# Performance work log

Measured on AMD Instinct MI355X. Metric: run time of the kernel, lower is better.

## Reference

```python
import jax, jax.numpy as jnp
import numpy as np

D_MODEL = 1024
D_INTERNAL = 256


def setup_inputs() -> dict:
    key = jax.random.key(0)
    ks = jax.random.split(key, 12)
    s = 0.02
    return {
        "x": jax.random.normal(ks[0], (4, 2048, D_MODEL), dtype=jnp.float32),
        "Wq": jax.random.normal(ks[1], (D_MODEL, D_INTERNAL), dtype=jnp.float32) * s,
        "bq": jnp.zeros((D_INTERNAL,), dtype=jnp.float32),
        "Wk": jax.random.normal(ks[2], (D_MODEL, D_INTERNAL), dtype=jnp.float32) * s,
        "bk": jnp.zeros((D_INTERNAL,), dtype=jnp.float32),
        "Wv": jax.random.normal(ks[3], (D_MODEL, D_MODEL), dtype=jnp.float32) * s,
        "bv": jnp.zeros((D_MODEL,), dtype=jnp.float32),
        "W1": jax.random.normal(ks[4], (D_MODEL, D_MODEL), dtype=jnp.float32) * s,
        "b1": jnp.zeros((D_MODEL,), dtype=jnp.float32),
        "W2": jax.random.normal(ks[5], (D_MODEL, D_MODEL), dtype=jnp.float32) * s,
        "b2": jnp.zeros((D_MODEL,), dtype=jnp.float32),
    }


def reference(x, Wq, bq, Wk, bk, Wv, bv, W1, b1, W2, b2):
    # x: [B, S, D]
    S = x.shape[-2]
    q = x @ Wq + bq            # [B, S, Di]
    k = x @ Wk + bk            # [B, S, Di]
    v = x @ Wv + bv            # [B, S, D]
    scale = 1.0 / jnp.sqrt(jnp.asarray(q.shape[-1], dtype=x.dtype))
    scores = jnp.einsum('bqd,bkd->bqk', q, k) * scale  # [B, S, S]
    causal_mask = jnp.triu(jnp.ones((S, S), dtype=bool), k=1)
    scores = jnp.where(causal_mask, -jnp.inf, scores)
    attn = jax.nn.softmax(scores, axis=-1)             # [B, S, S]
    attention = jnp.einsum('bqk,bkd->bqd', attn, v)    # [B, S, D]
    h = x + attention
    ff = jax.nn.relu(h @ W1 + b1) @ W2 + b2
    return h + ff, attn
```

## Files before the change

kernel.cpp:

```cpp
#include <hip/hip_runtime.h>
#include <hip/hip_bf16.h>

#define BM 128
#define BN 128

typedef __bf16 bf16x8 __attribute__((ext_vector_type(8)));
typedef float f32x4 __attribute__((ext_vector_type(4)));
typedef unsigned short u16;

__device__ __forceinline__ u16 f2bf(float f) {
    __bf16 b = (__bf16)f;
    return __builtin_bit_cast(u16, b);
}
__device__ __forceinline__ float bf2f(u16 u) {
    __bf16 b = __builtin_bit_cast(__bf16, u);
    return (float)b;
}

__device__ __forceinline__ void gload_lds16(const void* g, void* l) {
    __builtin_amdgcn_global_load_lds(
        (const __attribute__((address_space(1))) void*)g,
        (__attribute__((address_space(3))) void*)l,
        16, 0, 0);
}

template <int MODE>
__global__ __launch_bounds__(256)
void gemm_bt(const u16* __restrict__ A, int lda, long long a_bs,
             const u16* __restrict__ Bt, int ldb, long long b_bs,
             int Kdim, int ldc, long long c_bs,
             const float* __restrict__ bias, float scale,
             const void* __restrict__ resid, long long r_bs,
             void* __restrict__ out, int causal)
{
    int bx = blockIdx.x, by = blockIdx.y, bz = blockIdx.z;
    if (causal == 3) {
        const int t = blockIdx.x;
        int byy = (int)((sqrtf(8.f * (float)t + 1.f) - 1.f) * 0.5f);
        while ((byy + 1) * (byy + 2) / 2 <= t) byy++;
        while (byy * (byy + 1) / 2 > t) byy--;
        by = byy; bx = t - byy * (byy + 1) / 2; bz = blockIdx.y;
    }
    if (causal == 2 && bz >= 2) by = (int)gridDim.y - 1 - by;
    const int kend = (causal == 2) ? min(Kdim, (by + 1) * BM) : Kdim;

    A  += (long long)bz * a_bs;
    Bt += (long long)bz * b_bs;

    const int m0 = by * BM, n0 = bx * BN;
    const int tid = threadIdx.x;
    const int wave = tid >> 6, lane = tid & 63;
    const int wy = wave >> 1, wx = wave & 1;
    const int lr = lane >> 2, lc8 = (lane & 3) * 8;
    const int lane15 = lane & 15, kq = lane >> 4;

    __shared__ __align__(16) u16 As[2][BM * 32];
    __shared__ __align__(16) u16 Bs[2][BN * 32];

    f32x4 acc[4][4] = {};

    for (int k0 = 0; k0 < kend; k0 += 64) {
        __syncthreads();
        #pragma unroll
        for (int h = 0; h < 2; h++) {
            const int kh = k0 + h * 32 + lc8;
            #pragma unroll
            for (int it = 0; it < 2; it++) {
                const int row = wave * 16 + it * 64 + lr;
                gload_lds16(A  + (size_t)(m0 + row) * lda + kh,
                            &As[h][(wave * 16 + it * 64) * 32]);
                gload_lds16(Bt + (size_t)(n0 + row) * ldb + kh,
                            &Bs[h][(wave * 16 + it * 64) * 32]);
            }
        }
        __syncthreads();

        #pragma unroll
        for (int h = 0; h < 2; h++) {
            bf16x8 av[4], bv[4];
            #pragma unroll
            for (int i = 0; i < 4; i++)
                av[i] = *(const bf16x8*)&As[h][(wy * 64 + i * 16 + lane15) * 32 + kq * 8];
            #pragma unroll
            for (int j = 0; j < 4; j++)
                bv[j] = *(const bf16x8*)&Bs[h][(wx * 64 + j * 16 + lane15) * 32 + kq * 8];
            #pragma unroll
            for (int i = 0; i < 4; i++)
                #pragma unroll
                for (int j = 0; j < 4; j++)
                    acc[i][j] = __builtin_amdgcn_mfma_f32_16x16x32_bf16(av[i], bv[j], acc[i][j], 0, 0, 0);
        }
    }

    #pragma unroll
    for (int i = 0; i < 4; i++) {
        const int rl = m0 + wy * 64 + i * 16 + kq * 4;
        #pragma unroll
        for (int j = 0; j < 4; j++) {
            const int c = n0 + wx * 64 + j * 16 + lane15;
            #pragma unroll
            for (int rg = 0; rg < 4; rg++) {
                const int r = rl + rg;
                const size_t idx = (size_t)bz * c_bs + (size_t)r * ldc + c;
                const float v = acc[i][j][rg];
                if (MODE == 2) {
                    float p = __expf(v * scale);
                    if (c > r) p = 0.f;
                    ((u16*)out)[idx] = f2bf(p);
                } else if (MODE == 3) {
                    const u16* xr = (const u16*)resid;
                    const float linv = bias[(size_t)bz * 2048 + r];
                    const float h = bf2f(xr[(size_t)bz * r_bs + (size_t)r * ldc + c]) + v * linv;
                    ((u16*)out)[idx] = f2bf(h);
                }
            }
        }
    }
}

template <int MODE>
__global__ __launch_bounds__(512, 2)
void gemm_bt2(const u16* __restrict__ A, int lda,
              const u16* __restrict__ Bt, int ldb,
              int Kdim, int ldc,
              const float* __restrict__ bias,
              const void* __restrict__ resid,
              void* __restrict__ out)
{
    const int m0 = blockIdx.y * 256, n0 = blockIdx.x * 128;
    const int tid = threadIdx.x;
    const int wave = tid >> 6, lane = tid & 63;
    const int wr = wave >> 1, wc = wave & 1;
    const int lane15 = lane & 15, kq = lane >> 4;
    const int lr = lane >> 2;
    const int swzc8 = ((lane & 3) ^ ((lane >> 3) & 3)) * 8;
    const int lslot = lane15 * 32 + ((kq ^ ((lane15 >> 1) & 3)) * 8);

    __shared__ __align__(16) u16 As[3][2][256 * 32];
    __shared__ __align__(16) u16 Bs[3][2][128 * 32];

    f32x4 acc[4][4] = {};
    const int NT = Kdim >> 6;

    auto stage = [&](int buf, int t) {
        const int k0 = t << 6;
        #pragma unroll
        for (int h = 0; h < 2; h++) {
            const int kh = k0 + h * 32 + swzc8;
            #pragma unroll
            for (int it = 0; it < 2; it++) {
                const int row = wave * 16 + it * 128 + lr;
                gload_lds16(A + (size_t)(m0 + row) * lda + kh,
                            &As[buf][h][(wave * 16 + it * 128) * 32]);
            }
            gload_lds16(Bt + (size_t)(n0 + wave * 16 + lr) * ldb + kh,
                        &Bs[buf][h][(wave * 16) * 32]);
        }
    };

    stage(0, 0);
    stage(1, 1);

    int cur = 0;
    for (int t = 0; t < NT; t++) {
        if (t < NT - 1) asm volatile("s_waitcnt vmcnt(6) lgkmcnt(0)" ::: "memory");
        else            asm volatile("s_waitcnt vmcnt(0) lgkmcnt(0)" ::: "memory");
        __builtin_amdgcn_s_barrier();
        if (t + 2 < NT) {
            int tgt = cur + 2; if (tgt >= 3) tgt -= 3;
            stage(tgt, t + 2);
        }

        #pragma unroll
        for (int h = 0; h < 2; h++) {
            bf16x8 av[4], bv[4];
            #pragma unroll
            for (int i = 0; i < 4; i++)
                av[i] = *(const bf16x8*)&As[cur][h][(wr * 4 + i) * 512 + lslot];
            #pragma unroll
            for (int j = 0; j < 4; j++)
                bv[j] = *(const bf16x8*)&Bs[cur][h][(wc * 4 + j) * 512 + lslot];
            __builtin_amdgcn_s_setprio(1);
            #pragma unroll
            for (int i = 0; i < 4; i++)
                #pragma unroll
                for (int j = 0; j < 4; j++)
                    acc[i][j] = __builtin_amdgcn_mfma_f32_16x16x32_bf16(av[i], bv[j], acc[i][j], 0, 0, 0);
            __builtin_amdgcn_s_setprio(0);
        }
        cur++; if (cur == 3) cur = 0;
    }

    if (MODE == 6 && n0 >= 512) {
        u16* o = (u16*)resid;
        #pragma unroll
        for (int i = 0; i < 4; i++) {
            const int r = m0 + wr * 64 + i * 16 + kq * 4;
            const size_t base = (size_t)(r >> 11) * 1024 * 2048 + (r & 2047);
            #pragma unroll
            for (int j = 0; j < 4; j++) {
                const int c = n0 + wc * 64 + j * 16 + lane15;
                const float bj = bias[c];
                ushort4 pk;
                pk.x = f2bf(acc[i][j][0] + bj);
                pk.y = f2bf(acc[i][j][1] + bj);
                pk.z = f2bf(acc[i][j][2] + bj);
                pk.w = f2bf(acc[i][j][3] + bj);
                *(ushort4*)&o[base + (size_t)(c - 512) * 2048] = pk;
            }
        }
    } else {
        #pragma unroll
        for (int i = 0; i < 4; i++) {
            const int rl = m0 + wr * 64 + i * 16 + kq * 4;
            #pragma unroll
            for (int j = 0; j < 4; j++) {
                const int c = n0 + wc * 64 + j * 16 + lane15;
                const float bj = bias[c];
                #pragma unroll
                for (int rg = 0; rg < 4; rg++) {
                    const int r = rl + rg;
                    const size_t idx = (size_t)r * ldc + c;
                    const float v = acc[i][j][rg];
                    if (MODE == 4) {
                        ((u16*)out)[idx] = f2bf(fmaxf(v + bj, 0.f));
                    } else if (MODE == 5) {
                        const u16* hb = (const u16*)resid;
                        ((float*)out)[idx] = v + bj + bf2f(hb[idx]);
                    } else if (MODE == 6) {
                        ((u16*)out)[idx] = f2bf(v + bj);
                    }
                }
            }
        }
    }
}

__global__ __launch_bounds__(256)
void prep_x(const float* __restrict__ x, u16* __restrict__ xb)
{
    const int N4 = 8388608 / 4;
    for (int i = blockIdx.x * blockDim.x + threadIdx.x; i < N4; i += gridDim.x * blockDim.x) {
        const float4 v = ((const float4*)x)[i];
        ushort4 o;
        o.x = f2bf(v.x); o.y = f2bf(v.y); o.z = f2bf(v.z); o.w = f2bf(v.w);
        ((ushort4*)xb)[i] = o;
    }
}

__global__ __launch_bounds__(256)
void prep_w(const float* __restrict__ Wq, const float* __restrict__ bq,
            const float* __restrict__ Wk, const float* __restrict__ bk,
            const float* __restrict__ Wv, const float* __restrict__ bv,
            const float* __restrict__ b1, const float* __restrict__ b2,
            const float* __restrict__ W1, const float* __restrict__ W2,
            u16* __restrict__ WqkT, u16* __restrict__ WvT,
            u16* __restrict__ W1T, u16* __restrict__ W2T, float* __restrict__ biasv)
{
    const int bid = blockIdx.x, tid = threadIdx.x;
    if (bid == 896) {
        for (int t = tid; t < 3584; t += 256) {
            if (t < 512)       biasv[t] = (t < 256) ? bq[t] : bk[t - 256];
            else if (t < 1536) biasv[t] = bv[t - 512];
            else if (t < 2560) biasv[t] = b1[t - 1536];
            else               biasv[t] = b2[t - 2560];
        }
        return;
    }
    const float* src; u16* dst; int ld_src, kt, nt, nbase;
    if (bid < 128) {
        const int job = bid >> 6, t = bid & 63;
        src = job ? Wk : Wq; ld_src = 256;
        kt = t >> 2; nt = t & 3; nbase = job * 256 + nt * 64;
        dst = WqkT;
    } else {
        const int j = bid - 128, w = j >> 8, t = j & 255;
        src = (w == 0) ? Wv : (w == 1) ? W1 : W2; ld_src = 1024;
        kt = t >> 4; nt = t & 15; nbase = nt * 64;
        dst = (w == 0) ? WvT : (w == 1) ? W1T : W2T;
    }
    const int k0 = kt * 64;
    const int n0s = (ld_src == 256) ? (nbase & 255) : nbase;

    __shared__ float tile[64][65];
    const int ri = tid >> 4, j4 = (tid & 15) * 4;
    #pragma unroll
    for (int rr = 0; rr < 4; rr++) {
        const int i = ri + rr * 16;
        const float4 v = *(const float4*)&src[(size_t)(k0 + i) * ld_src + n0s + j4];
        tile[j4 + 0][i] = v.x;
        tile[j4 + 1][i] = v.y;
        tile[j4 + 2][i] = v.z;
        tile[j4 + 3][i] = v.w;
    }
    __syncthreads();
    const int n = tid >> 2, ks = (tid & 3) * 16;
    ushort4 o[4];
    #pragma unroll
    for (int c = 0; c < 4; c++) {
        o[c].x = f2bf(tile[n][ks + c * 4 + 0]);
        o[c].y = f2bf(tile[n][ks + c * 4 + 1]);
        o[c].z = f2bf(tile[n][ks + c * 4 + 2]);
        o[c].w = f2bf(tile[n][ks + c * 4 + 3]);
    }
    u16* drow = &dst[(size_t)(nbase + n) * 1024 + k0 + ks];
    #pragma unroll
    for (int c = 0; c < 4; c++) *(ushort4*)&drow[c * 4] = o[c];
}

__device__ __forceinline__ float wave_sum(float v) {
    #pragma unroll
    for (int off = 32; off > 0; off >>= 1) v += __shfl_xor(v, off, 64);
    return v;
}

__global__ __launch_bounds__(256)
void norm_kernel(const u16* __restrict__ attnb, float* __restrict__ attn,
                 float* __restrict__ linv)
{
    const int S = 2048;
    const int row = blockIdx.x;
    const int q = row & (S - 1);
    const int kpad = (q + 128) & ~127;
    const u16* brow = attnb + (size_t)row * S;
    float* srow = attn + (size_t)row * S;
    __shared__ float red[4];
    const int tid = threadIdx.x, wv = tid >> 6, ln = tid & 63;
    const int k = tid * 8;

    float vals[8];
    float lsum = 0.f;
    if (k < kpad) {
        const ushort4 a = *(const ushort4*)&brow[k];
        const ushort4 b = *(const ushort4*)&brow[k + 4];
        vals[0] = bf2f(a.x); vals[1] = bf2f(a.y); vals[2] = bf2f(a.z); vals[3] = bf2f(a.w);
        vals[4] = bf2f(b.x); vals[5] = bf2f(b.y); vals[6] = bf2f(b.z); vals[7] = bf2f(b.w);
        #pragma unroll
        for (int c = 0; c < 8; c++) lsum += vals[c];
    }
    lsum = wave_sum(lsum);
    if (ln == 0) red[wv] = lsum;
    __syncthreads();
    const float rinv = 1.f / (red[0] + red[1] + red[2] + red[3]);

    float4 o0 = {0.f, 0.f, 0.f, 0.f}, o1 = {0.f, 0.f, 0.f, 0.f};
    if (k < kpad) {
        o0 = make_float4(vals[0] * rinv, vals[1] * rinv, vals[2] * rinv, vals[3] * rinv);
        o1 = make_float4(vals[4] * rinv, vals[5] * rinv, vals[6] * rinv, vals[7] * rinv);
    }
    *(float4*)&srow[k] = o0;
    *(float4*)&srow[k + 4] = o1;
    if (tid == 0) linv[row] = rinv;
}

extern "C" void kernel_launch(void* const* d_in, const int* in_sizes, int n_in,
                              void* d_out, int out_size, void* d_ws, size_t ws_size,
                              hipStream_t stream)
{
    const float* x  = (const float*)d_in[0];
    const float* Wq = (const float*)d_in[1];
    const float* bq = (const float*)d_in[2];
    const float* Wk = (const float*)d_in[3];
    const float* bk = (const float*)d_in[4];
    const float* Wv = (const float*)d_in[5];
    const float* bv = (const float*)d_in[6];
    const float* W1 = (const float*)d_in[7];
    const float* b1 = (const float*)d_in[8];
    const float* W2 = (const float*)d_in[9];
    const float* b2 = (const float*)d_in[10];

    const int B = 4, S = 2048, D = 1024, BS = B * S;

    char* ws = (char*)d_ws;
    u16*   xb    = (u16*)(ws + 0);
    u16*   WqkT  = (u16*)(ws + 16777216);
    u16*   WvT   = (u16*)(ws + 17825792);
    u16*   W1T   = (u16*)(ws + 19922944);
    u16*   W2T   = (u16*)(ws + 22020096);
    float* biasv = (float*)(ws + 24117248);
    u16*   QK    = (u16*)(ws + 24133632);
    u16*   Vt    = (u16*)(ws + 32522240);
    u16*   attnb = (u16*)(ws + 49299456);
    float* linv  = (float*)(ws + 83886080);
    u16*   hb    = xb;
    u16*   ff1   = attnb;

    float* out0 = (float*)d_out;
    float* attn = out0 + (size_t)BS * D;

    const dim3 blk(256);

    prep_x<<<dim3(1024), blk, 0, stream>>>(x, xb);
    prep_w<<<dim3(897), blk, 0, stream>>>(Wq, bq, Wk, bk, Wv, bv, b1, b2, W1, W2,
                                          WqkT, WvT, W1T, W2T, biasv);

    gemm_bt2<6><<<dim3(12, 32), dim3(512), 0, stream>>>(
        xb, 1024, WqkT, 1024, 1024, 512, biasv, Vt, QK);

    gemm_bt<2><<<dim3(136, 4, 1), blk, 0, stream>>>(
        QK, 512, (long long)S * 512, QK + 256, 512, (long long)S * 512,
        256, S, (long long)S * S, nullptr, 0.0625f, nullptr, 0, attnb, 3);

    norm_kernel<<<dim3(BS), blk, 0, stream>>>(attnb, attn, linv);

    gemm_bt<3><<<dim3(8, 16, 4), blk, 0, stream>>>(
        attnb, S, (long long)S * S, Vt, S, (long long)D * S,
        S, D, (long long)S * D, linv, 1.f, xb, (long long)S * D, hb, 2);

    gemm_bt2<4><<<dim3(8, 32), dim3(512), 0, stream>>>(
        hb, 1024, W1T, 1024, 1024, 1024, biasv + 1536, nullptr, ff1);

    gemm_bt2<5><<<dim3(8, 32), dim3(512), 0, stream>>>(
        ff1, 1024, W2T, 1024, 1024, 1024, biasv + 2560, hb, out0);
}
```

Baseline: 347.5 us.

## Split GEMM K-tile staging into half-tile phases with finer-grained barriers

Restructures the GEMM main loop so each 64-wide K tile is processed as two 32-wide phases. Each phase issues its LDS reads, then the global-to-LDS loads for the matching half of tile t+2, waits with finer vmcnt counts, and runs its MFMAs. The last two tiles are peeled out of the loop. The aim is to interleave prefetch with compute more evenly and shorten vmcnt stalls, at the cost of two barriers per phase, so four per tile instead of one.

After: 330.5 us. 4.9% less time.

```diff
diff --git a/kernel.cpp b/kernel.cpp
--- a/kernel.cpp
+++ b/kernel.cpp
@@ -142,54 +142,64 @@
     f32x4 acc[4][4] = {};
     const int NT = Kdim >> 6;
 
-    auto stage = [&](int buf, int t) {
-        const int k0 = t << 6;
-        #pragma unroll
-        for (int h = 0; h < 2; h++) {
-            const int kh = k0 + h * 32 + swzc8;
-            #pragma unroll
-            for (int it = 0; it < 2; it++) {
-                const int row = wave * 16 + it * 128 + lr;
-                gload_lds16(A + (size_t)(m0 + row) * lda + kh,
-                            &As[buf][h][(wave * 16 + it * 128) * 32]);
-            }
-            gload_lds16(Bt + (size_t)(n0 + wave * 16 + lr) * ldb + kh,
-                        &Bs[buf][h][(wave * 16) * 32]);
-        }
+    auto stage_h = [&](int buf, int tt, int h) {
+        const int kh = (tt << 6) + h * 32 + swzc8;
+        #pragma unroll
+        for (int it = 0; it < 2; it++) {
+            const int row = wave * 16 + it * 128 + lr;
+            gload_lds16(A + (size_t)(m0 + row) * lda + kh,
+                        &As[buf][h][(wave * 16 + it * 128) * 32]);
+        }
+        gload_lds16(Bt + (size_t)(n0 + wave * 16 + lr) * ldb + kh,
+                    &Bs[buf][h][(wave * 16) * 32]);
     };
 
-    stage(0, 0);
-    stage(1, 1);
+#define PHASE(H, DO_STAGE, VM)                                                 \
+    {                                                                          \
+        bf16x8 av[4], bv[4];                                                   \
+        _Pragma("unroll")                                                      \
+        for (int i = 0; i < 4; i++)                                            \
+            av[i] = *(const bf16x8*)&As[cur][H][(wr * 4 + i) * 512 + lslot];   \
+        _Pragma("unroll")                                                      \
+        for (int j = 0; j < 4; j++)                                            \
+            bv[j] = *(const bf16x8*)&Bs[cur][H][(wc * 4 + j) * 512 + lslot];   \
+        if (DO_STAGE) {                                                        \
+            int tgt = cur + 2; if (tgt >= 3) tgt -= 3;                         \
+            stage_h(tgt, t + 2, H);                                            \
+        }                                                                      \
+        asm volatile("s_waitcnt vmcnt(" #VM ")" ::: "memory");                 \
+        __builtin_amdgcn_s_barrier();                                          \
+        asm volatile("s_waitcnt lgkmcnt(0)" ::: "memory");                     \
+        __builtin_amdgcn_s_setprio(1);                                         \
+        _Pragma("unroll")                                                      \
+        for (int i = 0; i < 4; i++)                                            \
+            _Pragma("unroll")                                                  \
+            for (int j = 0; j < 4; j++)                                        \
+                acc[i][j] = __builtin_amdgcn_mfma_f32_16x16x32_bf16(           \
+                    av[i], bv[j], acc[i][j], 0, 0, 0);                         \
+        __builtin_amdgcn_s_setprio(0);                                         \
+        __builtin_amdgcn_s_barrier();                                          \
+    }
+
+    stage_h(0, 0, 0); stage_h(0, 0, 1);
+    stage_h(1, 1, 0); stage_h(1, 1, 1);
+    asm volatile("s_waitcnt vmcnt(9)" ::: "memory");
+    __builtin_amdgcn_s_barrier();
 
     int cur = 0;
-    for (int t = 0; t < NT; t++) {
-        if (t < NT - 1) asm volatile("s_waitcnt vmcnt(6) lgkmcnt(0)" ::: "memory");
-        else            asm volatile("s_waitcnt vmcnt(0) lgkmcnt(0)" ::: "memory");
-        __builtin_amdgcn_s_barrier();
-        if (t + 2 < NT) {
-            int tgt = cur + 2; if (tgt >= 3) tgt -= 3;
-            stage(tgt, t + 2);
-        }
-
-        #pragma unroll
-        for (int h = 0; h < 2; h++) {
-            bf16x8 av[4], bv[4];
-            #pragma unroll
-            for (int i = 0; i < 4; i++)
-                av[i] = *(const bf16x8*)&As[cur][h][(wr * 4 + i) * 512 + lslot];
-            #pragma unroll
-            for (int j = 0; j < 4; j++)
-                bv[j] = *(const bf16x8*)&Bs[cur][h][(wc * 4 + j) * 512 + lslot];
-            __builtin_amdgcn_s_setprio(1);
-            #pragma unroll
-            for (int i = 0; i < 4; i++)
-                #pragma unroll
-                for (int j = 0; j < 4; j++)
-                    acc[i][j] = __builtin_amdgcn_mfma_f32_16x16x32_bf16(av[i], bv[j], acc[i][j], 0, 0, 0);
-            __builtin_amdgcn_s_setprio(0);
-        }
+    int t = 0;
+    for (; t < NT - 2; t++) {
+        PHASE(0, true, 9)
+        PHASE(1, true, 9)
         cur++; if (cur == 3) cur = 0;
     }
+    PHASE(0, false, 6)
+    PHASE(1, false, 3)
+    cur++; if (cur == 3) cur = 0;
+    t++;
+    PHASE(0, false, 0)
+    PHASE(1, false, 0)
+#undef PHASE
 
     if (MODE == 6 && n0 >= 512) {
         u16* o = (u16*)resid;
```

## Unroll dense GEMM K loop, split LDS buffers, pipeline ds_reads, swizzle workgroups for XCDs

Applied to the files above, without the earlier changes.

The gemm_bt2 kernel now has a compile-time K loop of 16 tiles that is fully unrolled. The triple buffers are split into separate static LDS arrays and all fragment loads for both K halves go out as inline ds_read_b128 up front. Partial lgkmcnt waits let the first MFMA group start while the second half's reads are still in flight. Workgroup IDs are also remapped in groups of 8, apparently to spread tiles across XCDs for L2 locality. The cost is a hardcoded K=1024 assumption, a larger unrolled code size and more register pressure.

New measurement: 303.6 us. 12.6% less time.

```diff
diff --git a/kernel.cpp b/kernel.cpp
--- a/kernel.cpp
+++ b/kernel.cpp
@@ -22,6 +22,14 @@
         (const __attribute__((address_space(1))) void*)g,
         (__attribute__((address_space(3))) void*)l,
         16, 0, 0);
+}
+
+__device__ __forceinline__ bf16x8 lds_read_b128(const u16* p) {
+    bf16x8 r;
+    const __attribute__((address_space(3))) u16* lp =
+        (const __attribute__((address_space(3))) u16*)p;
+    asm volatile("ds_read_b128 %0, %1" : "=v"(r) : "v"(lp));
+    return r;
 }
 
 template <int MODE>
@@ -122,12 +130,18 @@
 __global__ __launch_bounds__(512, 2)
 void gemm_bt2(const u16* __restrict__ A, int lda,
               const u16* __restrict__ Bt, int ldb,
-              int Kdim, int ldc,
+              int ldc,
               const float* __restrict__ bias,
               const void* __restrict__ resid,
               void* __restrict__ out)
 {
-    const int m0 = blockIdx.y * 256, n0 = blockIdx.x * 128;
+    constexpr int NT = 16;
+    const int gx = gridDim.x;
+    const int nwg = gx * (int)gridDim.y;
+    int lin = blockIdx.y * gx + blockIdx.x;
+    lin = (lin & 7) * (nwg >> 3) + (lin >> 3);
+    const int m0 = (lin / gx) * 256, n0 = (lin % gx) * 128;
+
     const int tid = threadIdx.x;
     const int wave = tid >> 6, lane = tid & 63;
     const int wr = wave >> 1, wc = wave & 1;
@@ -136,59 +150,80 @@
     const int swzc8 = ((lane & 3) ^ ((lane >> 3) & 3)) * 8;
     const int lslot = lane15 * 32 + ((kq ^ ((lane15 >> 1) & 3)) * 8);
 
-    __shared__ __align__(16) u16 As[3][2][256 * 32];
-    __shared__ __align__(16) u16 Bs[3][2][128 * 32];
+    __shared__ __align__(16) u16 As0[2][256 * 32];
+    __shared__ __align__(16) u16 As1[2][256 * 32];
+    __shared__ __align__(16) u16 As2[2][256 * 32];
+    __shared__ __align__(16) u16 Bs0[2][128 * 32];
+    __shared__ __align__(16) u16 Bs1[2][128 * 32];
+    __shared__ __align__(16) u16 Bs2[2][128 * 32];
 
     f32x4 acc[4][4] = {};
-    const int NT = Kdim >> 6;
-
-    auto stage = [&](int buf, int t) {
-        const int k0 = t << 6;
+
+    auto stage = [&](u16 (*Ad)[256 * 32], u16 (*Bd)[128 * 32], int tt) {
         #pragma unroll
         for (int h = 0; h < 2; h++) {
-            const int kh = k0 + h * 32 + swzc8;
+            const int kh = (tt << 6) + h * 32 + swzc8;
             #pragma unroll
             for (int it = 0; it < 2; it++) {
                 const int row = wave * 16 + it * 128 + lr;
                 gload_lds16(A + (size_t)(m0 + row) * lda + kh,
-                            &As[buf][h][(wave * 16 + it * 128) * 32]);
+                            &Ad[h][(wave * 16 + it * 128) * 32]);
             }
             gload_lds16(Bt + (size_t)(n0 + wave * 16 + lr) * ldb + kh,
-                        &Bs[buf][h][(wave * 16) * 32]);
+                        &Bd[h][(wave * 16) * 32]);
         }
     };
 
-    stage(0, 0);
-    stage(1, 1);
-
-    int cur = 0;
+    stage(As0, Bs0, 0);
+    stage(As1, Bs1, 1);
+
+    #pragma unroll
     for (int t = 0; t < NT; t++) {
-        if (t < NT - 1) asm volatile("s_waitcnt vmcnt(6) lgkmcnt(0)" ::: "memory");
-        else            asm volatile("s_waitcnt vmcnt(0) lgkmcnt(0)" ::: "memory");
+        u16 (*pAc)[256 * 32] = (t % 3 == 0) ? As0 : (t % 3 == 1) ? As1 : As2;
+        u16 (*pBc)[128 * 32] = (t % 3 == 0) ? Bs0 : (t % 3 == 1) ? Bs1 : Bs2;
+        if (t < NT - 1) asm volatile("s_waitcnt vmcnt(6)" ::: "memory");
+        else            asm volatile("s_waitcnt vmcnt(0)" ::: "memory");
         __builtin_amdgcn_s_barrier();
         if (t + 2 < NT) {
-            int tgt = cur + 2; if (tgt >= 3) tgt -= 3;
-            stage(tgt, t + 2);
-        }
-
-        #pragma unroll
-        for (int h = 0; h < 2; h++) {
-            bf16x8 av[4], bv[4];
-            #pragma unroll
-            for (int i = 0; i < 4; i++)
-                av[i] = *(const bf16x8*)&As[cur][h][(wr * 4 + i) * 512 + lslot];
+            const int tn = (t + 2) % 3;
+            u16 (*pAn)[256 * 32] = (tn == 0) ? As0 : (tn == 1) ? As1 : As2;
+            u16 (*pBn)[128 * 32] = (tn == 0) ? Bs0 : (tn == 1) ? Bs1 : Bs2;
+            stage(pAn, pBn, t + 2);
+        }
+
+        bf16x8 av0[4], bv0[4], av1[4], bv1[4];
+        #pragma unroll
+        for (int i = 0; i < 4; i++)
+            av0[i] = lds_read_b128(&pAc[0][(wr * 4 + i) * 512 + lslot]);
+        #pragma unroll
+        for (int j = 0; j < 4; j++)
+            bv0[j] = lds_read_b128(&pBc[0][(wc * 4 + j) * 512 + lslot]);
+        #pragma unroll
+        for (int i = 0; i < 4; i++)
+            av1[i] = lds_read_b128(&pAc[1][(wr * 4 + i) * 512 + lslot]);
+        #pragma unroll
+        for (int j = 0; j < 4; j++)
+            bv1[j] = lds_read_b128(&pBc[1][(wc * 4 + j) * 512 + lslot]);
+
+        asm volatile("s_waitcnt lgkmcnt(8)" ::: "memory");
+        __builtin_amdgcn_sched_barrier(0);
+        __builtin_amdgcn_s_setprio(1);
+        #pragma unroll
+        for (int i = 0; i < 4; i++)
             #pragma unroll
             for (int j = 0; j < 4; j++)
-                bv[j] = *(const bf16x8*)&Bs[cur][h][(wc * 4 + j) * 512 + lslot];
-            __builtin_amdgcn_s_setprio(1);
-            #pragma unroll
-            for (int i = 0; i < 4; i++)
-                #pragma unroll
-                for (int j = 0; j < 4; j++)
-                    acc[i][j] = __builtin_amdgcn_mfma_f32_16x16x32_bf16(av[i], bv[j], acc[i][j], 0, 0, 0);
-            __builtin_amdgcn_s_setprio(0);
-        }
-        cur++; if (cur == 3) cur = 0;
+                acc[i][j] = __builtin_amdgcn_mfma_f32_16x16x32_bf16(av0[i], bv0[j], acc[i][j], 0, 0, 0);
+        __builtin_amdgcn_s_setprio(0);
+
+        asm volatile("s_waitcnt lgkmcnt(0)" ::: "memory");
+        __builtin_amdgcn_sched_barrier(0);
+        __builtin_amdgcn_s_setprio(1);
+        #pragma unroll
+        for (int i = 0; i < 4; i++)
+            #pragma unroll
+            for (int j = 0; j < 4; j++)
+                acc[i][j] = __builtin_amdgcn_mfma_f32_16x16x32_bf16(av1[i], bv1[j], acc[i][j], 0, 0, 0);
+        __builtin_amdgcn_s_setprio(0);
     }
 
     if (MODE == 6 && n0 >= 512) {
@@ -395,7 +430,7 @@
                                           WqkT, WvT, W1T, W2T, biasv);
 
     gemm_bt2<6><<<dim3(12, 32), dim3(512), 0, stream>>>(
-        xb, 1024, WqkT, 1024, 1024, 512, biasv, Vt, QK);
+        xb, 1024, WqkT, 1024, 512, biasv, Vt, QK);
 
     gemm_bt<2><<<dim3(136, 4, 1), blk, 0, stream>>>(
         QK, 512, (long long)S * 512, QK + 256, 512, (long long)S * 512,
@@ -408,8 +443,8 @@
         S, D, (long long)S * D, linv, 1.f, xb, (long long)S * D, hb, 2);
 
     gemm_bt2<4><<<dim3(8, 32), dim3(512), 0, stream>>>(
-        hb, 1024, W1T, 1024, 1024, 1024, biasv + 1536, nullptr, ff1);
+        hb, 1024, W1T, 1024, 1024, biasv + 1536, nullptr, ff1);
 
     gemm_bt2<5><<<dim3(8, 32), dim3(512), 0, stream>>>(
-        ff1, 1024, W2T, 1024, 1024, 1024, biasv + 2560, hb, out0);
-}
+        ff1, 1024, W2T, 1024, 1024, biasv + 2560, hb, out0);
+}
```
